# Kernel optimization log

Measured on AMD Instinct MI355X. Metric: run time of the kernel, lower is better.

## Reference

```python
import jax, jax.numpy as jnp
import numpy as np

B, T, F, U = 64, 256, 64, 512  # batch, bid_sequence, features, lstm units


def setup_inputs() -> dict:
    key = jax.random.key(0)
    ks = jax.random.split(key, 8)
    sc = 0.05
    return {
        "inputs": jax.random.normal(ks[0], (B, T, F), jnp.float32),
        "kernel": jax.random.normal(ks[1], (F, 4 * U), jnp.float32) * sc,      # LSTM input kernel (i,f,c,o)
        "rec_kernel": jax.random.normal(ks[2], (U, 4 * U), jnp.float32) * sc,  # LSTM recurrent kernel
        "bias": jax.random.normal(ks[3], (4 * U,), jnp.float32) * sc,          # LSTM bias
        "att_W": jax.random.normal(ks[4], (T, T), jnp.float32) * sc,           # row t = weights of attention_denses[t] (first t cols used)
        "att_b": jax.random.normal(ks[5], (T,), jnp.float32) * sc,             # bias of attention_denses[t]
        "out_W": jax.random.normal(ks[6], (U,), jnp.float32) * sc,             # final Dense(1) kernel
        "out_b": jax.random.normal(ks[7], (), jnp.float32) * sc,               # final Dense(1) bias
    }


def reference(inputs, kernel, rec_kernel, bias, att_W, att_b, out_W, out_b):
    Bs, Ts, _ = inputs.shape
    Us = rec_kernel.shape[0]

    # ---- LSTM (keras LSTMCell, gate order i,f,c,o; sigmoid/tanh) ----
    xz = jnp.einsum('btf,fg->btg', inputs, kernel) + bias  # precompute input projection

    def step(carry, z):
        h, c = carry
        g = z + h @ rec_kernel
        i, f, gc, o = jnp.split(g, 4, axis=-1)
        c = jax.nn.sigmoid(f) * c + jax.nn.sigmoid(i) * jnp.tanh(gc)
        h = jax.nn.sigmoid(o) * jnp.tanh(c)
        return (h, c), h

    init = (jnp.zeros((Bs, Us), inputs.dtype), jnp.zeros((Bs, Us), inputs.dtype))
    _, hs = jax.lax.scan(step, init, jnp.swapaxes(xz, 0, 1))
    x = jnp.swapaxes(hs, 0, 1)  # (B, T, U)

    # ---- attention_loop ----
    # keras Attention([x[:t], [x[t]]]) softmaxes over a single key -> weights are
    # exactly 1, so attn output is x[t] tiled t times; transpose + Dense_t(1)
    # collapses to sum(att_W[t, :t]) * x[t] + att_b[t]. Step 0 passes x[0] through.
    t_idx = jnp.arange(Ts)
    tri = (t_idx[None, :] < t_idx[:, None]).astype(x.dtype)  # row t: first t cols valid
    coef = jnp.where(t_idx == 0, jnp.asarray(1.0, x.dtype), jnp.sum(att_W * tri, axis=1))
    shift = jnp.where(t_idx == 0, jnp.asarray(0.0, x.dtype), att_b)
    att = x * coef[None, :, None] + shift[None, :, None]  # (B, T, U)

    # ---- final Dense(1) + reshape + sigmoid ----
    return jax.nn.sigmoid(jnp.einsum('btu,u->bt', att, out_W) + out_b)  # (B, T)
```

## Files before the change

kernel.cpp:

```cpp
#include <hip/hip_runtime.h>
#include <hip/hip_bf16.h>
#include <string.h>

#define B_ 64
#define T_ 256
#define F_ 64
#define U_ 512
#define G4_ 2048
#define KTOT 576
#define KSTEPS 18

typedef __attribute__((ext_vector_type(8))) short short8;
typedef __attribute__((ext_vector_type(4))) float v4f;
typedef __attribute__((ext_vector_type(4))) int i4;
typedef unsigned short u16;

__device__ __forceinline__ float bf2f(u16 b) {
    unsigned int x = ((unsigned int)b) << 16;
    float f; memcpy(&f, &x, 4); return f;
}
__device__ __forceinline__ u16 f2bf(float f) {
    __hip_bfloat16 h = __float2bfloat16(f);
    u16 b; memcpy(&b, &h, 2); return b;
}
__device__ __forceinline__ float sigmoidf_(float x) { return 1.f / (1.f + __expf(-x)); }
__device__ __forceinline__ float tanhf_(float x) {
    float xc = fminf(15.f, fmaxf(-15.f, x));
    float e = __expf(2.f * xc);
    return (e - 1.f) / (e + 1.f);
}

__device__ __forceinline__ float ldany(const void* p, size_t i, int fg) {
    return fg ? ((const float*)p)[i] : bf2f(((const u16*)p)[i]);
}

#define WS_FLAG   0
#define WS_XB     64
#define WS_WP     2097216
#define WS_H2     4456512
#define WS_DOT    4718656
#define WS_BIASF  4784192
#define WS_ATTWF  4792384
#define WS_ATTBF  5054528
#define WS_OUTWF  5055552
#define WS_OUTBF  5057600
#define WS_NEED   5057920

__global__ __launch_bounds__(256) void detect(const unsigned int* __restrict__ w,
                                              int* __restrict__ flag) {
    __shared__ int votes;
    if (threadIdx.x == 0) votes = 0;
    __syncthreads();
    unsigned int v = w[threadIdx.x];
    int e = (v >> 7) & 0xFF;
    if (e >= 100 && e <= 135) atomicAdd(&votes, 1);
    __syncthreads();
    if (threadIdx.x == 0) *flag = (votes < 200) ? 1 : 0;
}

__global__ __launch_bounds__(256) void convert(const void* __restrict__ x,
                                               const void* __restrict__ bias,
                                               const void* __restrict__ attW,
                                               const void* __restrict__ attb,
                                               const void* __restrict__ outW,
                                               const void* __restrict__ outb,
                                               const int* __restrict__ flag,
                                               u16* __restrict__ xb,
                                               float* __restrict__ biasf,
                                               float* __restrict__ attWf,
                                               float* __restrict__ attbf,
                                               float* __restrict__ outWf,
                                               float* __restrict__ outbf,
                                               float* __restrict__ dot,
                                               unsigned int* __restrict__ h2z) {
    int fg = *flag;
    size_t i = (size_t)blockIdx.x * 256 + threadIdx.x;
    if (i < 1048576) {
        float v = ldany(x, i, fg);
        int b = (int)(i >> 14), t = (int)((i >> 6) & 255), f = (int)(i & 63);
        xb[((size_t)t * B_ + b) * F_ + f] = f2bf(v);
        return;
    }
    i -= 1048576;
    if (i < 2048)  { biasf[i] = ldany(bias, i, fg); return; }
    i -= 2048;
    if (i < 65536) { attWf[i] = ldany(attW, i, fg); return; }
    i -= 65536;
    if (i < 256)   { attbf[i] = ldany(attb, i, fg); return; }
    i -= 256;
    if (i < 512)   { outWf[i] = ldany(outW, i, fg); return; }
    i -= 512;
    if (i < 1)     { outbf[i] = ldany(outb, i, fg); return; }
    i -= 1;
    if (i < 16384) { dot[i] = 0.f; return; }
    i -= 16384;
    if (i < 32768) { h2z[i] = 0u; return; }
}

__global__ __launch_bounds__(256) void pack_w(const void* __restrict__ kin,
                                              const void* __restrict__ krec,
                                              const int* __restrict__ flag,
                                              u16* __restrict__ Wp) {
    int fg = *flag;
    int gid = blockIdx.x * 256 + threadIdx.x;
    int lane = gid & 63;
    int frag = gid >> 6;
    int nt = frag / KSTEPS;
    int ks = frag - nt * KSTEPS;
    int kbase = ks * 32 + (lane >> 4) * 8;
    int cp = nt * 16 + (lane & 15);
    int u = cp >> 2, gate = cp & 3;
    int C = gate * U_ + u;
    short8 v;
    for (int j = 0; j < 8; j++) {
        int k = kbase + j;
        float w = (k < F_) ? ldany(kin, (size_t)k * G4_ + C, fg)
                           : ldany(krec, (size_t)(k - F_) * G4_ + C, fg);
        v[j] = (short)f2bf(w);
    }
    *reinterpret_cast<short8*>(Wp + (size_t)gid * 8) = v;
}

__global__ __launch_bounds__(512, 1) void lstm_persist(const u16* __restrict__ xb,
                                                       const float* __restrict__ biasf,
                                                       const float* __restrict__ outWf,
                                                       const u16* __restrict__ Wp,
                                                       u16* __restrict__ h2,
                                                       float* __restrict__ dot) {
    __shared__ __align__(16) u16 stage[16 * 520];
    __shared__ float dp[32][16][9];

    int tid = threadIdx.x;
    int bid = blockIdx.x;
    int rg = bid & 3;
    int gu = bid >> 2;
    int w = tid >> 6, l = tid & 63;
    int nt = gu * 8 + w;

    short8 W[KSTEPS];
    #pragma unroll
    for (int ks = 0; ks < KSTEPS; ks++)
        W[ks] = *reinterpret_cast<const short8*>(Wp + ((size_t)(nt * KSTEPS + ks) * 64 + l) * 8);

    int arow = rg * 16 + (l & 15);
    int koff = (l >> 4) * 8;
    int plr = 2 * w + (l >> 5);
    int pcol = (l & 31) * 16;
    int e = l & 3;
    int j = (l >> 2) & 3;
    int erow = 4 * (l >> 4) + e;
    int unit = 4 * nt + j;
    float bia = biasf[0 * U_ + unit], bif = biasf[1 * U_ + unit];
    float big = biasf[2 * U_ + unit], bio = biasf[3 * U_ + unit];
    float wout = outWf[unit];
    float c = 0.f;

    for (int t = 0; t < T_; t++) {
        u16* hcur = h2 + (size_t)(t & 1) * (B_ * U_);
        const u16* hprev = h2 + (size_t)((t + 1) & 1) * (B_ * U_);
        unsigned int wtag = ((unsigned)(t >> 1) & 1u) ^ 1u;
        unsigned int rpat = ((((unsigned)(t - 1) >> 1) & 1u) ^ 1u) * 0x00010001u;

        const u16* xrow = xb + ((size_t)t * B_ + arow) * F_;
        short8 a0 = *reinterpret_cast<const short8*>(xrow + koff);
        short8 a1 = *reinterpret_cast<const short8*>(xrow + 32 + koff);
        v4f acc0 = {0.f, 0.f, 0.f, 0.f}, acc1 = {0.f, 0.f, 0.f, 0.f};
        acc0 = __builtin_amdgcn_mfma_f32_16x16x32_bf16(a0, W[0], acc0, 0, 0, 0);
        acc1 = __builtin_amdgcn_mfma_f32_16x16x32_bf16(a1, W[1], acc1, 0, 0, 0);
        __builtin_amdgcn_sched_barrier(0);

        i4 q0, q1;
        {
            const void* bp = (const void*)(hprev + (size_t)(rg * 16 + plr) * U_ + pcol);
            int spins = 0;
            for (;;) {
                asm volatile(
                    "global_load_dwordx4 %0, %2, off sc0 sc1\n\t"
                    "global_load_dwordx4 %1, %2, off offset:16 sc0 sc1\n\t"
                    "s_waitcnt vmcnt(0)"
                    : "=v"(q0), "=v"(q1) : "v"(bp) : "memory");
                if (t == 0) break;
                unsigned bad = 0;
                bad |= (((unsigned)q0[0]) ^ rpat) & 0x00010001u;
                bad |= (((unsigned)q0[1]) ^ rpat) & 0x00010001u;
                bad |= (((unsigned)q0[2]) ^ rpat) & 0x00010001u;
                bad |= (((unsigned)q0[3]) ^ rpat) & 0x00010001u;
                bad |= (((unsigned)q1[0]) ^ rpat) & 0x00010001u;
                bad |= (((unsigned)q1[1]) ^ rpat) & 0x00010001u;
                bad |= (((unsigned)q1[2]) ^ rpat) & 0x00010001u;
                bad |= (((unsigned)q1[3]) ^ rpat) & 0x00010001u;
                if (__ballot(bad == 0) == ~0ull) break;
                if (++spins > (1 << 14)) break;
                __builtin_amdgcn_s_sleep(2);
            }
        }
        *reinterpret_cast<i4*>(&stage[plr * 520 + pcol])     = q0;
        *reinterpret_cast<i4*>(&stage[plr * 520 + pcol + 8]) = q1;
        __syncthreads();

        #pragma unroll
        for (int ks = 2; ks < KSTEPS; ks += 2) {
            short8 ah0 = *reinterpret_cast<const short8*>(
                &stage[(l & 15) * 520 + (ks - 2) * 32 + koff]);
            short8 ah1 = *reinterpret_cast<const short8*>(
                &stage[(l & 15) * 520 + (ks - 1) * 32 + koff]);
            acc0 = __builtin_amdgcn_mfma_f32_16x16x32_bf16(ah0, W[ks],     acc0, 0, 0, 0);
            acc1 = __builtin_amdgcn_mfma_f32_16x16x32_bf16(ah1, W[ks + 1], acc1, 0, 0, 0);
        }
        v4f acc = acc0 + acc1;

        float g0 = acc[0], g1 = acc[1], g2 = acc[2], g3 = acc[3];
        {
            float t0 = __shfl_xor(g1, 1, 64);
            float t1 = __shfl_xor(g0, 1, 64);
            float t2 = __shfl_xor(g3, 1, 64);
            float t3 = __shfl_xor(g2, 1, 64);
            float b0 = ((0 ^ e) & 1) ? t0 : g0;
            float b1 = ((1 ^ e) & 1) ? t1 : g1;
            float b2 = ((2 ^ e) & 1) ? t2 : g2;
            float b3 = ((3 ^ e) & 1) ? t3 : g3;
            float u0 = __shfl_xor(b2, 2, 64);
            float u1 = __shfl_xor(b3, 2, 64);
            float u2 = __shfl_xor(b0, 2, 64);
            float u3 = __shfl_xor(b1, 2, 64);
            g0 = ((0 ^ e) & 2) ? u0 : b0;
            g1 = ((1 ^ e) & 2) ? u1 : b1;
            g2 = ((2 ^ e) & 2) ? u2 : b2;
            g3 = ((3 ^ e) & 2) ? u3 : b3;
        }

        {
            float ig = sigmoidf_(g0 + bia);
            float fg = sigmoidf_(g1 + bif);
            float gc = tanhf_(g2 + big);
            float og = sigmoidf_(g3 + bio);
            c = fg * c + ig * gc;
            float h = og * tanhf_(c);

            float hp = __shfl_xor(h, 4, 64);
            if (((l >> 2) & 1) == 0) {
                unsigned int pk = (unsigned int)(((unsigned)f2bf(h)  & 0xFFFEu) | wtag)
                                | ((unsigned int)(((unsigned)f2bf(hp) & 0xFFFEu) | wtag) << 16);
                void* sp = (void*)(hcur + (size_t)(rg * 16 + erow) * U_ + unit);
                asm volatile("global_store_dword %0, %1, off sc0 sc1"
                             :: "v"(sp), "v"(pk) : "memory");
            }

            float s = h * wout;
            s += __shfl_xor(s, 4, 64);
            s += __shfl_xor(s, 8, 64);
            if ((l & 12) == 0) dp[t & 31][erow][w] = s;
        }

        if ((t & 31) == 31) {
            __syncthreads();
            int t0_ = t - 31;
            int tt = tid >> 4, row = tid & 15;
            float sum = 0.f;
            #pragma unroll
            for (int ww = 0; ww < 8; ww++) sum += dp[tt][row][ww];
            atomicAdd(&dot[(size_t)(rg * 16 + row) * T_ + (t0_ + tt)], sum);
        }
    }
}

__global__ __launch_bounds__(256) void finale(const float* __restrict__ attWf,
                                              const float* __restrict__ attbf,
                                              const float* __restrict__ outWf,
                                              const float* __restrict__ outbf,
                                              const float* __restrict__ dot,
                                              const int* __restrict__ flag,
                                              void* __restrict__ out) {
    __shared__ float red[256];
    int t = blockIdx.x, tid = threadIdx.x;
    int fg = *flag;

    float v = (tid < t) ? attWf[(size_t)t * T_ + tid] : 0.f;
    red[tid] = v; __syncthreads();
    for (int s = 128; s > 0; s >>= 1) { if (tid < s) red[tid] += red[tid + s]; __syncthreads(); }
    float coef = (t == 0) ? 1.f : red[0];
    __syncthreads();
    red[tid] = outWf[tid] + outWf[tid + 256]; __syncthreads();
    for (int s = 128; s > 0; s >>= 1) { if (tid < s) red[tid] += red[tid + s]; __syncthreads(); }
    float sumW = red[0];

    float base = ((t == 0) ? 0.f : attbf[t]) * sumW + outbf[0];

    if (tid < B_) {
        float s = sigmoidf_(coef * dot[(size_t)tid * T_ + t] + base);
        size_t idx = (size_t)tid * T_ + t;
        if (fg) ((float*)out)[idx] = s;
        else    ((u16*)out)[idx] = f2bf(s);
    }
}

extern "C" void kernel_launch(void* const* d_in, const int* in_sizes, int n_in,
                              void* d_out, int out_size, void* d_ws, size_t ws_size,
                              hipStream_t stream) {
    const void* x    = d_in[0];
    const void* kin  = d_in[1];
    const void* krec = d_in[2];
    const void* bias = d_in[3];
    const void* attW = d_in[4];
    const void* attb = d_in[5];
    const void* outW = d_in[6];
    const void* outb = d_in[7];

    if (ws_size < (size_t)WS_NEED) return;

    char* ws = (char*)d_ws;
    int*   flag  = (int*)(ws + WS_FLAG);
    u16*   xb    = (u16*)(ws + WS_XB);
    u16*   Wp    = (u16*)(ws + WS_WP);
    u16*   h2    = (u16*)(ws + WS_H2);
    float* dot   = (float*)(ws + WS_DOT);
    float* biasf = (float*)(ws + WS_BIASF);
    float* attWf = (float*)(ws + WS_ATTWF);
    float* attbf = (float*)(ws + WS_ATTBF);
    float* outWf = (float*)(ws + WS_OUTWF);
    float* outbf = (float*)(ws + WS_OUTBF);

    detect<<<1, 256, 0, stream>>>((const unsigned int*)kin, flag);
    convert<<<4556, 256, 0, stream>>>(x, bias, attW, attb, outW, outb, flag,
                                      xb, biasf, attWf, attbf, outWf, outbf, dot,
                                      (unsigned int*)h2);
    pack_w<<<576, 256, 0, stream>>>(kin, krec, flag, Wp);
    lstm_persist<<<64, 512, 0, stream>>>(xb, biasf, outWf, Wp, h2, dot);
    finale<<<256, 256, 0, stream>>>(attWf, attbf, outWf, outbf, dot, flag, d_out);
}
```

Baseline: 608.9 us.

## Prefetch next-step hidden state speculatively and fold bias into MFMA accumulator

```diff
diff --git a/kernel.cpp b/kernel.cpp
--- a/kernel.cpp
+++ b/kernel.cpp
@@ -146,52 +146,75 @@
     int koff = (l >> 4) * 8;
     int plr = 2 * w + (l >> 5);
     int pcol = (l & 31) * 16;
+    size_t poff = (size_t)(rg * 16 + plr) * U_ + pcol;
     int e = l & 3;
     int j = (l >> 2) & 3;
     int erow = 4 * (l >> 4) + e;
     int unit = 4 * nt + j;
-    float bia = biasf[0 * U_ + unit], bif = biasf[1 * U_ + unit];
-    float big = biasf[2 * U_ + unit], bio = biasf[3 * U_ + unit];
+    int cp = nt * 16 + (l & 15);
+    float bc = biasf[(cp & 3) * U_ + (cp >> 2)];
     float wout = outWf[unit];
     float c = 0.f;
+
+    int tg = 1, te = 0;
+
+    i4 q0, q1;
+    {
+        const void* bp0 = (const void*)(h2 + (size_t)1 * (B_ * U_) + poff);
+        asm volatile(
+            "global_load_dwordx4 %0, %2, off sc0 sc1\n\t"
+            "global_load_dwordx4 %1, %2, off offset:16 sc0 sc1"
+            : "=v"(q0), "=v"(q1) : "v"(bp0) : "memory");
+    }
 
     for (int t = 0; t < T_; t++) {
         u16* hcur = h2 + (size_t)(t & 1) * (B_ * U_);
         const u16* hprev = h2 + (size_t)((t + 1) & 1) * (B_ * U_);
-        unsigned int wtag = ((unsigned)(t >> 1) & 1u) ^ 1u;
-        unsigned int rpat = ((((unsigned)(t - 1) >> 1) & 1u) ^ 1u) * 0x00010001u;
+        unsigned int pexp = (unsigned)(te & 1) | ((unsigned)((te >> 1) & 1) << 16);
 
         const u16* xrow = xb + ((size_t)t * B_ + arow) * F_;
         short8 a0 = *reinterpret_cast<const short8*>(xrow + koff);
         short8 a1 = *reinterpret_cast<const short8*>(xrow + 32 + koff);
-        v4f acc0 = {0.f, 0.f, 0.f, 0.f}, acc1 = {0.f, 0.f, 0.f, 0.f};
+        v4f acc0 = {bc, bc, bc, bc};
+        v4f acc1 = {0.f, 0.f, 0.f, 0.f};
         acc0 = __builtin_amdgcn_mfma_f32_16x16x32_bf16(a0, W[0], acc0, 0, 0, 0);
         acc1 = __builtin_amdgcn_mfma_f32_16x16x32_bf16(a1, W[1], acc1, 0, 0, 0);
+
+        asm volatile("s_waitcnt vmcnt(0)" : "+v"(q0), "+v"(q1) :: "memory");
         __builtin_amdgcn_sched_barrier(0);
 
-        i4 q0, q1;
-        {
-            const void* bp = (const void*)(hprev + (size_t)(rg * 16 + plr) * U_ + pcol);
-            int spins = 0;
-            for (;;) {
-                asm volatile(
-                    "global_load_dwordx4 %0, %2, off sc0 sc1\n\t"
-                    "global_load_dwordx4 %1, %2, off offset:16 sc0 sc1\n\t"
-                    "s_waitcnt vmcnt(0)"
-                    : "=v"(q0), "=v"(q1) : "v"(bp) : "memory");
-                if (t == 0) break;
-                unsigned bad = 0;
-                bad |= (((unsigned)q0[0]) ^ rpat) & 0x00010001u;
-                bad |= (((unsigned)q0[1]) ^ rpat) & 0x00010001u;
-                bad |= (((unsigned)q0[2]) ^ rpat) & 0x00010001u;
-                bad |= (((unsigned)q0[3]) ^ rpat) & 0x00010001u;
-                bad |= (((unsigned)q1[0]) ^ rpat) & 0x00010001u;
-                bad |= (((unsigned)q1[1]) ^ rpat) & 0x00010001u;
-                bad |= (((unsigned)q1[2]) ^ rpat) & 0x00010001u;
-                bad |= (((unsigned)q1[3]) ^ rpat) & 0x00010001u;
-                if (__ballot(bad == 0) == ~0ull) break;
-                if (++spins > (1 << 14)) break;
-                __builtin_amdgcn_s_sleep(2);
+        if (t != 0) {
+            unsigned bad = 0;
+            bad |= (((unsigned)q0[0]) ^ pexp) & 0x00010001u;
+            bad |= (((unsigned)q0[1]) ^ pexp) & 0x00010001u;
+            bad |= (((unsigned)q0[2]) ^ pexp) & 0x00010001u;
+            bad |= (((unsigned)q0[3]) ^ pexp) & 0x00010001u;
+            bad |= (((unsigned)q1[0]) ^ pexp) & 0x00010001u;
+            bad |= (((unsigned)q1[1]) ^ pexp) & 0x00010001u;
+            bad |= (((unsigned)q1[2]) ^ pexp) & 0x00010001u;
+            bad |= (((unsigned)q1[3]) ^ pexp) & 0x00010001u;
+            if (__ballot(bad == 0) != ~0ull) {
+                const void* bp = (const void*)(hprev + poff);
+                int spins = 0;
+                for (;;) {
+                    asm volatile(
+                        "global_load_dwordx4 %0, %2, off sc0 sc1\n\t"
+                        "global_load_dwordx4 %1, %2, off offset:16 sc0 sc1\n\t"
+                        "s_waitcnt vmcnt(0)"
+                        : "=v"(q0), "=v"(q1) : "v"(bp) : "memory");
+                    __builtin_amdgcn_sched_barrier(0);
+                    bad  = (((unsigned)q0[0]) ^ pexp) & 0x00010001u;
+                    bad |= (((unsigned)q0[1]) ^ pexp) & 0x00010001u;
+                    bad |= (((unsigned)q0[2]) ^ pexp) & 0x00010001u;
+                    bad |= (((unsigned)q0[3]) ^ pexp) & 0x00010001u;
+                    bad |= (((unsigned)q1[0]) ^ pexp) & 0x00010001u;
+                    bad |= (((unsigned)q1[1]) ^ pexp) & 0x00010001u;
+                    bad |= (((unsigned)q1[2]) ^ pexp) & 0x00010001u;
+                    bad |= (((unsigned)q1[3]) ^ pexp) & 0x00010001u;
+                    if (__ballot(bad == 0) == ~0ull) break;
+                    if (++spins > (1 << 14)) break;
+                    if (spins > 8) __builtin_amdgcn_s_sleep(1);
+                }
             }
         }
         *reinterpret_cast<i4*>(&stage[plr * 520 + pcol])     = q0;
@@ -230,17 +253,19 @@
         }
 
         {
-            float ig = sigmoidf_(g0 + bia);
-            float fg = sigmoidf_(g1 + bif);
-            float gc = tanhf_(g2 + big);
-            float og = sigmoidf_(g3 + bio);
+            float ig = sigmoidf_(g0);
+            float fg = sigmoidf_(g1);
+            float gc = tanhf_(g2);
+            float og = sigmoidf_(g3);
             c = fg * c + ig * gc;
             float h = og * tanhf_(c);
 
             float hp = __shfl_xor(h, 4, 64);
             if (((l >> 2) & 1) == 0) {
-                unsigned int pk = (unsigned int)(((unsigned)f2bf(h)  & 0xFFFEu) | wtag)
-                                | ((unsigned int)(((unsigned)f2bf(hp) & 0xFFFEu) | wtag) << 16);
+                unsigned int b0t = (unsigned)(tg & 1);
+                unsigned int b1t = (unsigned)((tg >> 1) & 1);
+                unsigned int pk = (unsigned int)(((unsigned)f2bf(h)  & 0xFFFEu) | b0t)
+                                | ((unsigned int)(((unsigned)f2bf(hp) & 0xFFFEu) | b1t) << 16);
                 void* sp = (void*)(hcur + (size_t)(rg * 16 + erow) * U_ + unit);
                 asm volatile("global_store_dword %0, %1, off sc0 sc1"
                              :: "v"(sp), "v"(pk) : "memory");
@@ -261,6 +286,17 @@
             for (int ww = 0; ww < 8; ww++) sum += dp[tt][row][ww];
             atomicAdd(&dot[(size_t)(rg * 16 + row) * T_ + (t0_ + tt)], sum);
         }
+
+        if (t < T_ - 1) {
+            const void* bpn = (const void*)(hcur + poff);
+            asm volatile(
+                "global_load_dwordx4 %0, %2, off sc0 sc1\n\t"
+                "global_load_dwordx4 %1, %2, off offset:16 sc0 sc1"
+                : "=v"(q0), "=v"(q1) : "v"(bpn) : "memory");
+        }
+
+        te = tg;
+        tg = (tg == 3) ? 1 : tg + 1;
     }
 }
 
```

Measured after the change: 1.047 ms. 1.72x slower.

## Give each wave two gate tiles and halve persistent LSTM grid to 32 blocks

Applied to the files above, without the earlier changes.

```diff
diff --git a/kernel.cpp b/kernel.cpp
--- a/kernel.cpp
+++ b/kernel.cpp
@@ -13,6 +13,7 @@
 typedef __attribute__((ext_vector_type(8))) short short8;
 typedef __attribute__((ext_vector_type(4))) float v4f;
 typedef __attribute__((ext_vector_type(4))) int i4;
+typedef __attribute__((ext_vector_type(2))) int i2;
 typedef unsigned short u16;
 
 __device__ __forceinline__ float bf2f(u16 b) {
@@ -135,12 +136,14 @@
     int rg = bid & 3;
     int gu = bid >> 2;
     int w = tid >> 6, l = tid & 63;
-    int nt = gu * 8 + w;
-
-    short8 W[KSTEPS];
+    int nt0 = gu * 16 + 2 * w;
+
+    short8 W0[KSTEPS], W1[KSTEPS];
     #pragma unroll
-    for (int ks = 0; ks < KSTEPS; ks++)
-        W[ks] = *reinterpret_cast<const short8*>(Wp + ((size_t)(nt * KSTEPS + ks) * 64 + l) * 8);
+    for (int ks = 0; ks < KSTEPS; ks++) {
+        W0[ks] = *reinterpret_cast<const short8*>(Wp + ((size_t)(nt0 * KSTEPS + ks) * 64 + l) * 8);
+        W1[ks] = *reinterpret_cast<const short8*>(Wp + ((size_t)((nt0 + 1) * KSTEPS + ks) * 64 + l) * 8);
+    }
 
     int arow = rg * 16 + (l & 15);
     int koff = (l >> 4) * 8;
@@ -149,11 +152,14 @@
     int e = l & 3;
     int j = (l >> 2) & 3;
     int erow = 4 * (l >> 4) + e;
-    int unit = 4 * nt + j;
-    float bia = biasf[0 * U_ + unit], bif = biasf[1 * U_ + unit];
-    float big = biasf[2 * U_ + unit], bio = biasf[3 * U_ + unit];
-    float wout = outWf[unit];
-    float c = 0.f;
+    int unit0 = 4 * nt0 + j;
+    int unit1 = unit0 + 4;
+    int cp0 = nt0 * 16 + (l & 15);
+    int cp1 = cp0 + 16;
+    float bc0 = biasf[(cp0 & 3) * U_ + (cp0 >> 2)];
+    float bc1 = biasf[(cp1 & 3) * U_ + (cp1 >> 2)];
+    float wout0 = outWf[unit0], wout1 = outWf[unit1];
+    float c0 = 0.f, c1 = 0.f;
 
     for (int t = 0; t < T_; t++) {
         u16* hcur = h2 + (size_t)(t & 1) * (B_ * U_);
@@ -164,9 +170,14 @@
         const u16* xrow = xb + ((size_t)t * B_ + arow) * F_;
         short8 a0 = *reinterpret_cast<const short8*>(xrow + koff);
         short8 a1 = *reinterpret_cast<const short8*>(xrow + 32 + koff);
-        v4f acc0 = {0.f, 0.f, 0.f, 0.f}, acc1 = {0.f, 0.f, 0.f, 0.f};
-        acc0 = __builtin_amdgcn_mfma_f32_16x16x32_bf16(a0, W[0], acc0, 0, 0, 0);
-        acc1 = __builtin_amdgcn_mfma_f32_16x16x32_bf16(a1, W[1], acc1, 0, 0, 0);
+        v4f acc0A = {bc0, bc0, bc0, bc0};
+        v4f acc0B = {0.f, 0.f, 0.f, 0.f};
+        v4f acc1A = {bc1, bc1, bc1, bc1};
+        v4f acc1B = {0.f, 0.f, 0.f, 0.f};
+        acc0A = __builtin_amdgcn_mfma_f32_16x16x32_bf16(a0, W0[0], acc0A, 0, 0, 0);
+        acc0B = __builtin_amdgcn_mfma_f32_16x16x32_bf16(a1, W0[1], acc0B, 0, 0, 0);
+        acc1A = __builtin_amdgcn_mfma_f32_16x16x32_bf16(a0, W1[0], acc1A, 0, 0, 0);
+        acc1B = __builtin_amdgcn_mfma_f32_16x16x32_bf16(a1, W1[1], acc1B, 0, 0, 0);
         __builtin_amdgcn_sched_barrier(0);
 
         i4 q0, q1;
@@ -204,13 +215,17 @@
                 &stage[(l & 15) * 520 + (ks - 2) * 32 + koff]);
             short8 ah1 = *reinterpret_cast<const short8*>(
                 &stage[(l & 15) * 520 + (ks - 1) * 32 + koff]);
-            acc0 = __builtin_amdgcn_mfma_f32_16x16x32_bf16(ah0, W[ks],     acc0, 0, 0, 0);
-            acc1 = __builtin_amdgcn_mfma_f32_16x16x32_bf16(ah1, W[ks + 1], acc1, 0, 0, 0);
-        }
-        v4f acc = acc0 + acc1;
-
-        float g0 = acc[0], g1 = acc[1], g2 = acc[2], g3 = acc[3];
+            acc0A = __builtin_amdgcn_mfma_f32_16x16x32_bf16(ah0, W0[ks],     acc0A, 0, 0, 0);
+            acc0B = __builtin_amdgcn_mfma_f32_16x16x32_bf16(ah1, W0[ks + 1], acc0B, 0, 0, 0);
+            acc1A = __builtin_amdgcn_mfma_f32_16x16x32_bf16(ah0, W1[ks],     acc1A, 0, 0, 0);
+            acc1B = __builtin_amdgcn_mfma_f32_16x16x32_bf16(ah1, W1[ks + 1], acc1B, 0, 0, 0);
+        }
+        v4f accT0 = acc0A + acc0B;
+        v4f accT1 = acc1A + acc1B;
+
+        float h0v, h1v;
         {
+            float g0 = accT0[0], g1 = accT0[1], g2 = accT0[2], g3 = accT0[3];
             float t0 = __shfl_xor(g1, 1, 64);
             float t1 = __shfl_xor(g0, 1, 64);
             float t2 = __shfl_xor(g3, 1, 64);
@@ -227,26 +242,59 @@
             g1 = ((1 ^ e) & 2) ? u1 : b1;
             g2 = ((2 ^ e) & 2) ? u2 : b2;
             g3 = ((3 ^ e) & 2) ? u3 : b3;
-        }
-
+            float ig = sigmoidf_(g0);
+            float fg = sigmoidf_(g1);
+            float gc = tanhf_(g2);
+            float og = sigmoidf_(g3);
+            c0 = fg * c0 + ig * gc;
+            h0v = og * tanhf_(c0);
+        }
         {
-            float ig = sigmoidf_(g0 + bia);
-            float fg = sigmoidf_(g1 + bif);
-            float gc = tanhf_(g2 + big);
-            float og = sigmoidf_(g3 + bio);
-            c = fg * c + ig * gc;
-            float h = og * tanhf_(c);
-
-            float hp = __shfl_xor(h, 4, 64);
-            if (((l >> 2) & 1) == 0) {
-                unsigned int pk = (unsigned int)(((unsigned)f2bf(h)  & 0xFFFEu) | wtag)
-                                | ((unsigned int)(((unsigned)f2bf(hp) & 0xFFFEu) | wtag) << 16);
-                void* sp = (void*)(hcur + (size_t)(rg * 16 + erow) * U_ + unit);
-                asm volatile("global_store_dword %0, %1, off sc0 sc1"
-                             :: "v"(sp), "v"(pk) : "memory");
+            float g0 = accT1[0], g1 = accT1[1], g2 = accT1[2], g3 = accT1[3];
+            float t0 = __shfl_xor(g1, 1, 64);
+            float t1 = __shfl_xor(g0, 1, 64);
+            float t2 = __shfl_xor(g3, 1, 64);
+            float t3 = __shfl_xor(g2, 1, 64);
+            float b0 = ((0 ^ e) & 1) ? t0 : g0;
+            float b1 = ((1 ^ e) & 1) ? t1 : g1;
+            float b2 = ((2 ^ e) & 1) ? t2 : g2;
+            float b3 = ((3 ^ e) & 1) ? t3 : g3;
+            float u0 = __shfl_xor(b2, 2, 64);
+            float u1 = __shfl_xor(b3, 2, 64);
+            float u2 = __shfl_xor(b0, 2, 64);
+            float u3 = __shfl_xor(b1, 2, 64);
+            g0 = ((0 ^ e) & 2) ? u0 : b0;
+            g1 = ((1 ^ e) & 2) ? u1 : b1;
+            g2 = ((2 ^ e) & 2) ? u2 : b2;
+            g3 = ((3 ^ e) & 2) ? u3 : b3;
+            float ig = sigmoidf_(g0);
+            float fg = sigmoidf_(g1);
+            float gc = tanhf_(g2);
+            float og = sigmoidf_(g3);
+            c1 = fg * c1 + ig * gc;
+            h1v = og * tanhf_(c1);
+        }
+
+        {
+            float hp0 = __shfl_xor(h0v, 4, 64);
+            float hp1 = __shfl_xor(h1v, 4, 64);
+            unsigned int pk0 = (unsigned int)(((unsigned)f2bf(h0v) & 0xFFFEu) | wtag)
+                             | ((unsigned int)(((unsigned)f2bf(hp0) & 0xFFFEu) | wtag) << 16);
+            unsigned int pk1 = (unsigned int)(((unsigned)f2bf(h1v) & 0xFFFEu) | wtag)
+                             | ((unsigned int)(((unsigned)f2bf(hp1) & 0xFFFEu) | wtag) << 16);
+            unsigned int xv = (j & 2) ? pk0 : pk1;
+            unsigned int yv = (unsigned int)__shfl_xor((int)xv, 8, 64);
+            if ((j & 1) == 0) {
+                i2 dv;
+                int ub;
+                if ((j & 2) == 0) { dv[0] = (int)pk0; dv[1] = (int)yv; ub = 4 * nt0; }
+                else              { dv[0] = (int)yv;  dv[1] = (int)pk1; ub = 4 * nt0 + 4; }
+                void* sp = (void*)(hcur + (size_t)(rg * 16 + erow) * U_ + ub);
+                asm volatile("global_store_dwordx2 %0, %1, off sc0 sc1"
+                             :: "v"(sp), "v"(dv) : "memory");
             }
 
-            float s = h * wout;
+            float s = h0v * wout0 + h1v * wout1;
             s += __shfl_xor(s, 4, 64);
             s += __shfl_xor(s, 8, 64);
             if ((l & 12) == 0) dp[t & 31][erow][w] = s;
@@ -325,6 +373,6 @@
                                       xb, biasf, attWf, attbf, outWf, outbf, dot,
                                       (unsigned int*)h2);
     pack_w<<<576, 256, 0, stream>>>(kin, krec, flag, Wp);
-    lstm_persist<<<64, 512, 0, stream>>>(xb, biasf, outWf, Wp, h2, dot);
+    lstm_persist<<<32, 512, 0, stream>>>(xb, biasf, outWf, Wp, h2, dot);
     finale<<<256, 256, 0, stream>>>(attWf, attbf, outWf, outbf, dot, flag, d_out);
 }
```

Result: slower. 739.8 us (+21.5%).

## Split recurrent h wait into two halves and overlap second with MFMAs

Applied to the files above, without the earlier changes.

```diff
diff --git a/kernel.cpp b/kernel.cpp
--- a/kernel.cpp
+++ b/kernel.cpp
@@ -130,6 +130,9 @@
     __shared__ __align__(16) u16 stage[16 * 520];
     __shared__ float dp[32][16][9];
 
+    const unsigned long long UPPER_MASK = 0xFFFF0000FFFF0000ULL;
+    const unsigned long long LOWER_MASK = 0x0000FFFF0000FFFFULL;
+
     int tid = threadIdx.x;
     int bid = blockIdx.x;
     int rg = bid & 3;
@@ -146,10 +149,10 @@
     int koff = (l >> 4) * 8;
     int plr = 2 * w + (l >> 5);
     int pcol = (l & 31) * 16;
+    int upper_lane = ((l & 31) >= 16);
     int e = l & 3;
-    int j = (l >> 2) & 3;
     int erow = 4 * (l >> 4) + e;
-    int unit = 4 * nt + j;
+    int unit = 4 * nt + ((l >> 2) & 3);
     float bia = biasf[0 * U_ + unit], bif = biasf[1 * U_ + unit];
     float big = biasf[2 * U_ + unit], bio = biasf[3 * U_ + unit];
     float wout = outWf[unit];
@@ -160,6 +163,7 @@
         const u16* hprev = h2 + (size_t)((t + 1) & 1) * (B_ * U_);
         unsigned int wtag = ((unsigned)(t >> 1) & 1u) ^ 1u;
         unsigned int rpat = ((((unsigned)(t - 1) >> 1) & 1u) ^ 1u) * 0x00010001u;
+        const void* bp = (const void*)(hprev + (size_t)(rg * 16 + plr) * U_ + pcol);
 
         const u16* xrow = xb + ((size_t)t * B_ + arow) * F_;
         short8 a0 = *reinterpret_cast<const short8*>(xrow + koff);
@@ -171,7 +175,6 @@
 
         i4 q0, q1;
         {
-            const void* bp = (const void*)(hprev + (size_t)(rg * 16 + plr) * U_ + pcol);
             int spins = 0;
             for (;;) {
                 asm volatile(
@@ -189,7 +192,7 @@
                 bad |= (((unsigned)q1[1]) ^ rpat) & 0x00010001u;
                 bad |= (((unsigned)q1[2]) ^ rpat) & 0x00010001u;
                 bad |= (((unsigned)q1[3]) ^ rpat) & 0x00010001u;
-                if (__ballot(bad == 0) == ~0ull) break;
+                if ((__ballot(bad == 0) | UPPER_MASK) == ~0ull) break;
                 if (++spins > (1 << 14)) break;
                 __builtin_amdgcn_s_sleep(2);
             }
@@ -198,8 +201,65 @@
         *reinterpret_cast<i4*>(&stage[plr * 520 + pcol + 8]) = q1;
         __syncthreads();
 
+        asm volatile(
+            "global_load_dwordx4 %0, %2, off sc0 sc1\n\t"
+            "global_load_dwordx4 %1, %2, off offset:16 sc0 sc1"
+            : "=v"(q0), "=v"(q1) : "v"(bp) : "memory");
+
         #pragma unroll
-        for (int ks = 2; ks < KSTEPS; ks += 2) {
+        for (int ks = 2; ks < 10; ks += 2) {
+            short8 ah0 = *reinterpret_cast<const short8*>(
+                &stage[(l & 15) * 520 + (ks - 2) * 32 + koff]);
+            short8 ah1 = *reinterpret_cast<const short8*>(
+                &stage[(l & 15) * 520 + (ks - 1) * 32 + koff]);
+            acc0 = __builtin_amdgcn_mfma_f32_16x16x32_bf16(ah0, W[ks],     acc0, 0, 0, 0);
+            acc1 = __builtin_amdgcn_mfma_f32_16x16x32_bf16(ah1, W[ks + 1], acc1, 0, 0, 0);
+        }
+
+        asm volatile("s_waitcnt vmcnt(0)" : "+v"(q0), "+v"(q1) :: "memory");
+        __builtin_amdgcn_sched_barrier(0);
+
+        if (t != 0) {
+            unsigned bad = 0;
+            bad |= (((unsigned)q0[0]) ^ rpat) & 0x00010001u;
+            bad |= (((unsigned)q0[1]) ^ rpat) & 0x00010001u;
+            bad |= (((unsigned)q0[2]) ^ rpat) & 0x00010001u;
+            bad |= (((unsigned)q0[3]) ^ rpat) & 0x00010001u;
+            bad |= (((unsigned)q1[0]) ^ rpat) & 0x00010001u;
+            bad |= (((unsigned)q1[1]) ^ rpat) & 0x00010001u;
+            bad |= (((unsigned)q1[2]) ^ rpat) & 0x00010001u;
+            bad |= (((unsigned)q1[3]) ^ rpat) & 0x00010001u;
+            if ((__ballot(bad == 0) | LOWER_MASK) != ~0ull) {
+                int spins = 0;
+                for (;;) {
+                    asm volatile(
+                        "global_load_dwordx4 %0, %2, off sc0 sc1\n\t"
+                        "global_load_dwordx4 %1, %2, off offset:16 sc0 sc1\n\t"
+                        "s_waitcnt vmcnt(0)"
+                        : "=v"(q0), "=v"(q1) : "v"(bp) : "memory");
+                    __builtin_amdgcn_sched_barrier(0);
+                    bad  = (((unsigned)q0[0]) ^ rpat) & 0x00010001u;
+                    bad |= (((unsigned)q0[1]) ^ rpat) & 0x00010001u;
+                    bad |= (((unsigned)q0[2]) ^ rpat) & 0x00010001u;
+                    bad |= (((unsigned)q0[3]) ^ rpat) & 0x00010001u;
+                    bad |= (((unsigned)q1[0]) ^ rpat) & 0x00010001u;
+                    bad |= (((unsigned)q1[1]) ^ rpat) & 0x00010001u;
+                    bad |= (((unsigned)q1[2]) ^ rpat) & 0x00010001u;
+                    bad |= (((unsigned)q1[3]) ^ rpat) & 0x00010001u;
+                    if ((__ballot(bad == 0) | LOWER_MASK) == ~0ull) break;
+                    if (++spins > (1 << 14)) break;
+                    __builtin_amdgcn_s_sleep(2);
+                }
+            }
+        }
+        if (upper_lane) {
+            *reinterpret_cast<i4*>(&stage[plr * 520 + pcol])     = q0;
+            *reinterpret_cast<i4*>(&stage[plr * 520 + pcol + 8]) = q1;
+        }
+        __syncthreads();
+
+        #pragma unroll
+        for (int ks = 10; ks < KSTEPS; ks += 2) {
             short8 ah0 = *reinterpret_cast<const short8*>(
                 &stage[(l & 15) * 520 + (ks - 2) * 32 + koff]);
             short8 ah1 = *reinterpret_cast<const short8*>(
```

Measured after the change: 670.6 us. +10.1%, slower.
